# Optimization experiments

Hardware: AMD Instinct MI355X
Metric: run time of the kernel (lower is better)

The kernel has to match this reference:

```python
import jax, jax.numpy as jnp
import numpy as np

N, D, K = 8192, 2048, 10000
EPS = 1e-12
COMMITMENT_COST = 0.25


def _l2_normalize(v, axis):
    # matches torch F.normalize(p=2): v / max(||v||, eps)
    n = jnp.linalg.norm(v, axis=axis, keepdims=True)
    return v / jnp.maximum(n, EPS)


def setup_inputs() -> dict:
    key = jax.random.key(0)
    kx, kw = jax.random.split(key)
    x = jax.random.normal(kx, (N, D), dtype=jnp.float32)
    # nn.Embedding weight initialized uniform(0, 3) per the module
    weight = jax.random.uniform(kw, (K, D), dtype=jnp.float32, minval=0.0, maxval=3.0)
    return {"x": x, "weight": weight}


def reference(x, weight):
    # --- get_code_indices ---
    xn = _l2_normalize(x, axis=1)          # [N, D]
    wn = _l2_normalize(weight, axis=1)     # [K, D]
    # ||xn||^2 + ||wn||^2 - 2 xn . wn  -> [N, K]
    distances = (
        jnp.sum(xn * xn, axis=1, keepdims=True)
        + jnp.sum(wn * wn, axis=1)
        - 2.0 * jnp.matmul(xn, wn.T)
    )
    encoding_indices = jnp.argmin(distances, axis=1)  # [N]
    # --- quantize (gathers the UN-normalized codebook, as in the module) ---
    quantized = weight[encoding_indices]              # [N, D]
    # --- training losses ---
    q_latent_loss = jnp.mean((quantized - jax.lax.stop_gradient(x)) ** 2)
    e_latent_loss = jnp.mean((x - jax.lax.stop_gradient(quantized)) ** 2)
    loss = q_latent_loss + COMMITMENT_COST * e_latent_loss
    # straight-through estimator
    quantized = x + jax.lax.stop_gradient(quantized - x)
    return quantized, loss, encoding_indices
```

## Files before the change

kernel.cpp:

```cpp
#include <hip/hip_runtime.h>
#include <math.h>

typedef unsigned short ushort_t;
typedef short short8 __attribute__((ext_vector_type(8)));
typedef float f32x4  __attribute__((ext_vector_type(4)));

#define N_ROWS 8192
#define D_DIM  2048
#define K_CODES 10000
#define EPSF   1e-12f

#define BMT 256
#define BKT 64
#define NT_K 32
#define MTILES 32
#define NTILES 40
#define NGROUP 320

#define BAND_ADD  2e-5f
#define FBIG 1e30f

__device__ __forceinline__ unsigned short f2bf(float f) {
  unsigned u = __float_as_uint(f);
  unsigned r = (u + 0x7fffu + ((u >> 16) & 1u)) >> 16;
  return (unsigned short)r;
}
__device__ __forceinline__ float bf2f(unsigned short h) {
  return __uint_as_float(((unsigned)h) << 16);
}

__device__ __forceinline__ void stage16(const ushort_t* g, ushort_t* l) {
  __builtin_amdgcn_global_load_lds(
      (const __attribute__((address_space(1))) unsigned int*)g,
      (__attribute__((address_space(3))) unsigned int*)l, 16, 0, 0);
}

__device__ __forceinline__ float block_reduce_sum(float v) {
  #pragma unroll
  for (int o = 32; o > 0; o >>= 1) v += __shfl_down(v, o, 64);
  __shared__ float ls[4];
  int lane = threadIdx.x & 63;
  int wid  = threadIdx.x >> 6;
  if (lane == 0) ls[wid] = v;
  __syncthreads();
  v = (threadIdx.x < 4) ? ls[threadIdx.x] : 0.0f;
  if (wid == 0) {
    v += __shfl_down(v, 2, 64);
    v += __shfl_down(v, 1, 64);
  }
  __syncthreads();
  return v;
}

__global__ __launch_bounds__(256) void norm_hi_kernel(
    const float* __restrict__ src, ushort_t* __restrict__ hi,
    float* __restrict__ sq_out, float* __restrict__ inv_out,
    float* __restrict__ hn_out, float* __restrict__ ln_out)
{
  int row = blockIdx.x;
  int tid = threadIdx.x;
  const float* rp = src + (size_t)row * D_DIM;
  float4 v0 = *(const float4*)(rp + tid * 8);
  float4 v1 = *(const float4*)(rp + tid * 8 + 4);
  float s = v0.x*v0.x + v0.y*v0.y + v0.z*v0.z + v0.w*v0.w
          + v1.x*v1.x + v1.y*v1.y + v1.z*v1.z + v1.w*v1.w;
  s = block_reduce_sum(s);
  __shared__ float sh_inv;
  if (tid == 0) sh_inv = 1.0f / fmaxf(sqrtf(s), EPSF);
  __syncthreads();
  float inv = sh_inv;

  float xs[8] = {v0.x, v0.y, v0.z, v0.w, v1.x, v1.y, v1.z, v1.w};
  unsigned short hb[8];
  float t = 0.0f, th = 0.0f, tl = 0.0f;
  #pragma unroll
  for (int i = 0; i < 8; ++i) {
    float xn = xs[i] * inv;
    t += xn * xn;
    unsigned short h = f2bf(xn);
    hb[i] = h;
    float hf = bf2f(h);
    th += hf * hf;
    float l = xn - hf;
    tl += l * l;
  }
  *(short8*)(hi + (size_t)row * D_DIM + tid * 8) = *(short8*)hb;
  t  = block_reduce_sum(t);
  if (tid == 0) sq_out[row] = t;
  th = block_reduce_sum(th);
  if (tid == 0) hn_out[row] = sqrtf(th);
  tl = block_reduce_sum(tl);
  if (tid == 0) { ln_out[row] = sqrtf(tl); inv_out[row] = inv; }
}

__global__ __launch_bounds__(256) void wmax_kernel(
    const float* __restrict__ whn, const float* __restrict__ wln,
    float* __restrict__ wmax_out)
{
  int tid = threadIdx.x;
  float mh = 0.0f, ml = 0.0f;
  for (int k = tid; k < K_CODES; k += 256) {
    mh = fmaxf(mh, whn[k]);
    ml = fmaxf(ml, wln[k]);
  }
  __shared__ float sh[256], sl[256];
  sh[tid] = mh; sl[tid] = ml;
  __syncthreads();
  #pragma unroll
  for (int o = 128; o > 0; o >>= 1) {
    if (tid < o) {
      sh[tid] = fmaxf(sh[tid], sh[tid + o]);
      sl[tid] = fmaxf(sl[tid], sl[tid + o]);
    }
    __syncthreads();
  }
  if (tid == 0) { wmax_out[0] = sh[0]; wmax_out[1] = sl[0]; }
}

#define LEXLT(da, ia, db, ib) ((da) < (db) || ((da) == (db) && (ia) < (ib)))


#define READ_A(mh) { \
  _Pragma("unroll") for (int mi = 0; mi < 4; ++mi) { \
    af[mi][0] = *(const short8*)(aP0 + bo + (mh)*8192 + mi*1024); \
    af[mi][1] = *(const short8*)(aP1 + bo + (mh)*8192 + mi*1024); } }

#define READ_B(nh, DST) { \
  _Pragma("unroll") for (int ni = 0; ni < 2; ++ni) { \
    DST[ni][0] = *(const short8*)(bP0 + bo + (nh)*8192 + ni*1024); \
    DST[ni][1] = *(const short8*)(bP1 + bo + (nh)*8192 + ni*1024); } }

#define MFMA_Q(mh, nh, BF) { \
  _Pragma("unroll") for (int mi = 0; mi < 4; ++mi) \
  _Pragma("unroll") for (int ni = 0; ni < 2; ++ni) \
  _Pragma("unroll") for (int kc = 0; kc < 2; ++kc) \
    acc[(mh)*4+mi][(nh)*2+ni] = __builtin_amdgcn_mfma_f32_16x16x32_bf16( \
        af[mi][kc], BF[ni][kc], acc[(mh)*4+mi][(nh)*2+ni], 0, 0, 0); }

#define STAGE_A(NB, HH, KKO) { \
  stage16(Ah + (size_t)(row0 + (HH)*128 + prow0) * D_DIM + (KKO) + lsl, \
          &lA[0][0] + (NB)*16384 + (HH)*8192 + c0*512); \
  stage16(Ah + (size_t)(row0 + (HH)*128 + prow1) * D_DIM + (KKO) + lsl, \
          &lA[0][0] + (NB)*16384 + (HH)*8192 + c0*512 + 512); }

#define STAGE_B(NB, HH, KKO) { \
  int r0_ = col0 + (HH)*128 + prow0; r0_ = r0_ < K_CODES ? r0_ : K_CODES - 1; \
  int r1_ = col0 + (HH)*128 + prow1; r1_ = r1_ < K_CODES ? r1_ : K_CODES - 1; \
  stage16(Bh + (size_t)r0_ * D_DIM + (KKO) + lsl, \
          &lB[0][0] + (NB)*16384 + (HH)*8192 + c0*512); \
  stage16(Bh + (size_t)r1_ * D_DIM + (KKO) + lsl, \
          &lB[0][0] + (NB)*16384 + (HH)*8192 + c0*512 + 512); }

__global__ __launch_bounds__(512, 2) void dist_top2_kernel(
    const ushort_t* __restrict__ Ah, const ushort_t* __restrict__ Bh,
    const float* __restrict__ wsq,
    float* __restrict__ p1d, int* __restrict__ p1i, float* __restrict__ p2d)
{
  __shared__ ushort_t lA[2][16384];
  __shared__ ushort_t lB[2][16384];

  const int tid  = threadIdx.x;
  const int lane = tid & 63;
  const int w8   = tid >> 6;
  const int wr   = w8 >> 2;
  const int wc   = w8 & 3;
  const int t16  = lane & 15;
  const int h4   = lane >> 4;

  int bid = blockIdx.x;
  int xcd = bid & 7, l = bid >> 3;
  int ch = l >> 5;
  int wl = l & 31;
  const int mtile = (xcd & 1) * 16 + (wl & 15);
  const int ntile = (xcd >> 1) * 10 + ch * 2 + (wl >> 4);
  const int row0 = mtile * BMT;
  const int col0 = ntile * BMT;

  const int sub  = lane >> 3;
  const int lsl  = ((lane & 7) ^ sub) * 8;
  const int c0   = w8 * 2;
  const int prow0 = c0 * 8 + sub;
  const int prow1 = prow0 + 8;

  const int rA = wr * 64 + t16;
  const ushort_t* aP0 = &lA[0][rA * 64 + ((h4     ^ (rA & 7)) * 8)];
  const ushort_t* aP1 = &lA[0][rA * 64 + (((4+h4) ^ (rA & 7)) * 8)];
  const int rB = wc * 32 + t16;
  const ushort_t* bP0 = &lB[0][rB * 64 + ((h4     ^ (rB & 7)) * 8)];
  const ushort_t* bP1 = &lB[0][rB * 64 + (((4+h4) ^ (rB & 7)) * 8)];

  f32x4 acc[8][4];
  #pragma unroll
  for (int m = 0; m < 8; ++m)
    #pragma unroll
    for (int n = 0; n < 4; ++n) acc[m][n] = (f32x4){0.f, 0.f, 0.f, 0.f};

  STAGE_A(0, 0, 0);
  STAGE_B(0, 0, 0);
  STAGE_B(0, 1, 0);
  STAGE_A(0, 1, 0);
  __syncthreads();

  short8 af[4][2], bfr0[2][2], bfr1[2][2];

  for (int kt = 0; kt < NT_K; ++kt) {
    const int bo   = (kt & 1) * 16384;
    const int nb   = (kt + 1) & 1;
    const bool hn  = (kt + 1 < NT_K);
    const int kk   = (kt + 1) * BKT;

    if (hn) {
      STAGE_A(nb, 0, kk);
      STAGE_B(nb, 0, kk);
      STAGE_B(nb, 1, kk);
      STAGE_A(nb, 1, kk);
    }

    READ_A(0);
    READ_B(0, bfr0);
    __builtin_amdgcn_s_setprio(1);
    MFMA_Q(0, 0, bfr0);
    __builtin_amdgcn_s_setprio(0);
    READ_B(1, bfr1);
    __builtin_amdgcn_s_setprio(1);
    MFMA_Q(0, 1, bfr1);
    __builtin_amdgcn_s_setprio(0);
    READ_A(1);
    __builtin_amdgcn_s_setprio(1);
    MFMA_Q(1, 1, bfr1);
    MFMA_Q(1, 0, bfr0);
    __builtin_amdgcn_s_setprio(0);

    __syncthreads();
  }

  float wsqr[4]; int colr[4];
  #pragma unroll
  for (int n = 0; n < 4; ++n) {
    int col = col0 + ((n & 2) ? 128 : 0) + wc * 32 + ((n & 1) ? 16 : 0) + t16;
    colr[n] = col;
    wsqr[n] = (col < K_CODES) ? wsq[col] : FBIG * 10.0f;
  }
  #pragma unroll
  for (int m = 0; m < 8; ++m) {
    int rloc = ((m & 4) ? 128 : 0) + wr * 64 + (m & 3) * 16 + h4 * 4;
    #pragma unroll
    for (int j = 0; j < 4; ++j) {
      #pragma unroll
      for (int half = 0; half < 2; ++half) {
        int na = half * 2, nb2 = na + 1;
        float da = wsqr[na]  - 2.0f * acc[m][na][j];  int ia = colr[na];
        float db = wsqr[nb2] - 2.0f * acc[m][nb2][j]; int ib = colr[nb2];
        float d1, d2; int i1;
        if (LEXLT(db, ib, da, ia)) { d1 = db; i1 = ib; d2 = da; }
        else                       { d1 = da; i1 = ia; d2 = db; }
        #pragma unroll
        for (int off = 1; off < 16; off <<= 1) {
          float od1 = __shfl_xor(d1, off, 64);
          int   oi1 = __shfl_xor(i1, off, 64);
          float od2 = __shfl_xor(d2, off, 64);
          if (LEXLT(od1, oi1, d1, i1)) { d2 = fminf(d1, od2); d1 = od1; i1 = oi1; }
          else                         { d2 = fminf(od1, d2); }
        }
        if (t16 == 0) {
          int grow = row0 + rloc + j;
          int gid = ntile * 8 + half * 4 + wc;
          size_t o = (size_t)grow * NGROUP + gid;
          p1d[o] = d1; p1i[o] = i1; p2d[o] = d2;
        }
      }
    }
  }
}

__global__ __launch_bounds__(256) void refine_kernel(
    const float* __restrict__ x, const float* __restrict__ w,
    const float* __restrict__ xsq, const float* __restrict__ xinv,
    const float* __restrict__ xhn, const float* __restrict__ xln,
    const float* __restrict__ wsq, const float* __restrict__ winv,
    const float* __restrict__ whn, const float* __restrict__ wln,
    const float* __restrict__ wmax,
    const float* __restrict__ p1d, const int* __restrict__ p1i,
    const float* __restrict__ p2d,
    int* __restrict__ idx_out, float* __restrict__ idxf_out)
{
  const int wv   = threadIdx.x >> 6;
  const int lane = threadIdx.x & 63;
  const int row  = blockIdx.x * 4 + wv;

  const float xs = xsq[row], xh = xhn[row], xl = xln[row];
  const float whm = wmax[0], wlm = wmax[1];
  const float eps_max = 2.0f * (xl * whm + xh * wlm + xl * wlm) + BAND_ADD;

  float gd1[5], gd2[5], geps[5];
  int   gi1[5];
  float tmin = FBIG;
  float bmind = FBIG; int bmink = 0x7fffffff;
  #pragma unroll
  for (int s = 0; s < 5; ++s) {
    size_t o = (size_t)row * NGROUP + lane + 64 * s;
    float d1 = p1d[o]; int i1 = p1i[o]; float d2 = p2d[o];
    int is = i1 < K_CODES ? i1 : K_CODES - 1;
    float e1 = 2.0f * (xl * whn[is] + xh * wln[is] + xl * wln[is]) + BAND_ADD;
    gd1[s] = d1; gi1[s] = i1; gd2[s] = d2; geps[s] = e1;
    tmin = fminf(tmin, d1 + e1);
    if (d1 < bmind || (d1 == bmind && i1 < bmink)) { bmind = d1; bmink = i1; }
  }
  #pragma unroll
  for (int off = 1; off < 64; off <<= 1) tmin = fminf(tmin, __shfl_xor(tmin, off, 64));
  const float T = tmin;

  #pragma unroll
  for (int off = 1; off < 64; off <<= 1) {
    float od = __shfl_xor(bmind, off, 64);
    int   ok = __shfl_xor(bmink, off, 64);
    if (od < bmind || (od == bmind && ok < bmink)) { bmind = od; bmink = ok; }
  }
  const int kfirst = bmink;

  unsigned long long ms[5], mc[5];
  int ncand = 0, nscan = 0;
  #pragma unroll
  for (int s = 0; s < 5; ++s) {
    bool scan = (gd2[s] - eps_max <= T);
    bool cand = !scan && (gd1[s] - geps[s] <= T);
    ms[s] = __ballot(scan); mc[s] = __ballot(cand);
    nscan += __popcll(ms[s]); ncand += __popcll(mc[s]);
  }
  if (nscan == 0 && ncand == 1) {
    if (lane == 0) { idx_out[row] = kfirst; idxf_out[row] = (float)kfirst; }
    return;
  }

  const float4* xr4 = (const float4*)(x + (size_t)row * D_DIM);
  const float xiv = xinv[row];
  float4 xv[8];
  #pragma unroll
  for (int j = 0; j < 8; ++j) {
    float4 v = xr4[lane + 64 * j];
    v.x *= xiv; v.y *= xiv; v.z *= xiv; v.w *= xiv;
    xv[j] = v;
  }

  float bd = INFINITY; int bi = 0x7fffffff;
  auto refine = [&](int k) {
    const float4* wr4 = (const float4*)(w + (size_t)k * D_DIM);
    const float wiv = winv[k];
    float a = 0.0f;
    #pragma unroll
    for (int j = 0; j < 8; ++j) {
      float4 wvv = wr4[lane + 64 * j];
      a += xv[j].x * (wvv.x * wiv) + xv[j].y * (wvv.y * wiv)
         + xv[j].z * (wvv.z * wiv) + xv[j].w * (wvv.w * wiv);
    }
    #pragma unroll
    for (int off = 32; off > 0; off >>= 1) a += __shfl_xor(a, off, 64);
    float df = (xs + wsq[k]) - 2.0f * a;
    if (df < bd || (df == bd && k < bi)) { bd = df; bi = k; }
  };

  if (kfirst < K_CODES) refine(kfirst);

  #pragma unroll
  for (int s = 0; s < 5; ++s) {
    unsigned long long m = mc[s];
    while (m) {
      int lsrc = __ffsll(m) - 1; m &= m - 1;
      int k = __shfl(gi1[s], lsrc, 64);
      if (k == kfirst || k >= K_CODES) continue;
      float a1d = __shfl(gd1[s],  lsrc, 64);
      float a1e = __shfl(geps[s], lsrc, 64);
      if (a1d - a1e <= bd + BAND_ADD) refine(k);
    }
    m = ms[s];
    while (m) {
      int lsrc = __ffsll(m) - 1; m &= m - 1;
      float a2d = __shfl(gd2[s], lsrc, 64);
      if (a2d - eps_max > bd + BAND_ADD) continue;
      int k0 = (lsrc + 64 * s) * 32;
      for (int kk = 0; kk < 32; ++kk) {
        int k = k0 + kk;
        if (k < K_CODES) refine(k);
      }
    }
  }

  if (lane == 0) { idx_out[row] = bi; idxf_out[row] = (float)bi; }
}

__global__ __launch_bounds__(256) void gather_kernel(
    const float* __restrict__ x, const float* __restrict__ w,
    const int* __restrict__ idx, float* __restrict__ out,
    float* __restrict__ lpart)
{
  int row = blockIdx.x;
  int tid = threadIdx.x;
  int id = idx[row];
  const float4* wr_ = (const float4*)(w + (size_t)id * D_DIM);
  const float4* xr  = (const float4*)(x + (size_t)row * D_DIM);
  float4* outr = (float4*)(out + (size_t)row * D_DIM);
  float s = 0.0f;
  #pragma unroll
  for (int t = 0; t < 2; ++t) {
    int e = tid + t * 256;
    float4 wv = wr_[e], xv = xr[e];
    outr[e] = wv;
    float d0 = wv.x - xv.x, d1 = wv.y - xv.y, d2 = wv.z - xv.z, d3 = wv.w - xv.w;
    s += d0 * d0 + d1 * d1 + d2 * d2 + d3 * d3;
  }
  s = block_reduce_sum(s);
  if (tid == 0) lpart[row] = s;
}

__global__ __launch_bounds__(256) void loss_kernel(const float* __restrict__ lpart,
                                                   float* __restrict__ loss_out)
{
  int tid = threadIdx.x;
  double s = 0.0;
  for (int t = tid; t < N_ROWS; t += 256) s += (double)lpart[t];
  __shared__ double sd[256];
  sd[tid] = s;
  __syncthreads();
  #pragma unroll
  for (int o = 128; o > 0; o >>= 1) {
    if (tid < o) sd[tid] += sd[tid + o];
    __syncthreads();
  }
  if (tid == 0)
    loss_out[0] = (float)(1.25 * sd[0] / (double)((size_t)N_ROWS * (size_t)D_DIM));
}

extern "C" void kernel_launch(void* const* d_in, const int* in_sizes, int n_in,
                              void* d_out, int out_size, void* d_ws, size_t ws_size,
                              hipStream_t stream) {
  const float* x = (const float*)d_in[0];
  const float* w = (const float*)d_in[1];
  float* out = (float*)d_out;
  char*  ws  = (char*)d_ws;

  size_t off = 0;
  auto alloc = [&](size_t bytes) {
    size_t o = off;
    off = (off + bytes + 255) & ~(size_t)255;
    return o;
  };
  const size_t szA1 = (size_t)N_ROWS * D_DIM * 2;
  const size_t szB1 = (size_t)K_CODES * D_DIM * 2;
  const size_t szP  = (size_t)NGROUP * N_ROWS * 4;

  ushort_t* Bh = (ushort_t*)(ws + alloc(szB1));
  float* wsq  = (float*)(ws + alloc((size_t)K_CODES * 4));
  float* winv = (float*)(ws + alloc((size_t)K_CODES * 4));
  float* whn  = (float*)(ws + alloc((size_t)K_CODES * 4));
  float* wln  = (float*)(ws + alloc((size_t)K_CODES * 4));
  float* wmax = (float*)(ws + alloc(2 * 4));
  float* xsq  = (float*)(ws + alloc((size_t)N_ROWS * 4));
  float* xinv = (float*)(ws + alloc((size_t)N_ROWS * 4));
  float* xhn  = (float*)(ws + alloc((size_t)N_ROWS * 4));
  float* xln  = (float*)(ws + alloc((size_t)N_ROWS * 4));
  float* p1d  = (float*)(ws + alloc(szP));
  int*   p1i  = (int*)  (ws + alloc(szP));
  float* p2d  = (float*)(ws + alloc(szP));
  int*   idx  = (int*)  (ws + alloc((size_t)N_ROWS * 4));
  float* lpart = (float*)(ws + alloc((size_t)N_ROWS * 4));

  ushort_t* Ahp;
  if (ws_size >= off + szA1) {
    Ahp = (ushort_t*)(ws + alloc(szA1));
  } else {
    Ahp = (ushort_t*)out;
  }

  float* loss_out = out + (size_t)N_ROWS * D_DIM;
  float* idxf_out = loss_out + 1;

  norm_hi_kernel<<<N_ROWS, 256, 0, stream>>>(x, Ahp, xsq, xinv, xhn, xln);
  norm_hi_kernel<<<K_CODES, 256, 0, stream>>>(w, Bh, wsq, winv, whn, wln);
  wmax_kernel<<<1, 256, 0, stream>>>(whn, wln, wmax);
  dist_top2_kernel<<<MTILES * NTILES, 512, 0, stream>>>(
      Ahp, Bh, wsq, p1d, p1i, p2d);
  refine_kernel<<<N_ROWS / 4, 256, 0, stream>>>(
      x, w, xsq, xinv, xhn, xln, wsq, winv, whn, wln, wmax,
      p1d, p1i, p2d, idx, idxf_out);
  gather_kernel<<<N_ROWS, 256, 0, stream>>>(x, w, idx, out, lpart);
  loss_kernel<<<1, 256, 0, stream>>>(lpart, loss_out);
}
```

Baseline: 785.5 us.

## Replace 256x256 double-buffered GEMM tile with simple single-buffered 128x128 tile

The distance GEMM kernel moves from 256x256 tiles with 512 threads, double-buffered LDS, setprio interleaving and an XCD-aware block swizzle to 128x128 tiles with 256 threads, a single LDS buffer and two barriers per k-step. The candidate output layout is remapped so that each 128-column tile still yields four groups, keeping NGROUP at 320. The intent is to raise occupancy and the number of blocks, but the change drops the global-load/compute overlap, lowers the arithmetic intensity per tile, and removes the L2-locality swizzle.

```diff
diff --git a/kernel.cpp b/kernel.cpp
--- a/kernel.cpp
+++ b/kernel.cpp
@@ -10,11 +10,11 @@
 #define K_CODES 10000
 #define EPSF   1e-12f
 
-#define BMT 256
+#define BMT 128
 #define BKT 64
-#define NT_K 32
-#define MTILES 32
-#define NTILES 40
+#define KT_N 32
+#define MT 64
+#define NT 80
 #define NGROUP 320
 
 #define BAND_ADD  2e-5f
@@ -120,137 +120,91 @@
 #define LEXLT(da, ia, db, ib) ((da) < (db) || ((da) == (db) && (ia) < (ib)))
 
 
-#define READ_A(mh) { \
-  _Pragma("unroll") for (int mi = 0; mi < 4; ++mi) { \
-    af[mi][0] = *(const short8*)(aP0 + bo + (mh)*8192 + mi*1024); \
-    af[mi][1] = *(const short8*)(aP1 + bo + (mh)*8192 + mi*1024); } }
-
-#define READ_B(nh, DST) { \
-  _Pragma("unroll") for (int ni = 0; ni < 2; ++ni) { \
-    DST[ni][0] = *(const short8*)(bP0 + bo + (nh)*8192 + ni*1024); \
-    DST[ni][1] = *(const short8*)(bP1 + bo + (nh)*8192 + ni*1024); } }
-
-#define MFMA_Q(mh, nh, BF) { \
-  _Pragma("unroll") for (int mi = 0; mi < 4; ++mi) \
-  _Pragma("unroll") for (int ni = 0; ni < 2; ++ni) \
-  _Pragma("unroll") for (int kc = 0; kc < 2; ++kc) \
-    acc[(mh)*4+mi][(nh)*2+ni] = __builtin_amdgcn_mfma_f32_16x16x32_bf16( \
-        af[mi][kc], BF[ni][kc], acc[(mh)*4+mi][(nh)*2+ni], 0, 0, 0); }
-
-#define STAGE_A(NB, HH, KKO) { \
-  stage16(Ah + (size_t)(row0 + (HH)*128 + prow0) * D_DIM + (KKO) + lsl, \
-          &lA[0][0] + (NB)*16384 + (HH)*8192 + c0*512); \
-  stage16(Ah + (size_t)(row0 + (HH)*128 + prow1) * D_DIM + (KKO) + lsl, \
-          &lA[0][0] + (NB)*16384 + (HH)*8192 + c0*512 + 512); }
-
-#define STAGE_B(NB, HH, KKO) { \
-  int r0_ = col0 + (HH)*128 + prow0; r0_ = r0_ < K_CODES ? r0_ : K_CODES - 1; \
-  int r1_ = col0 + (HH)*128 + prow1; r1_ = r1_ < K_CODES ? r1_ : K_CODES - 1; \
-  stage16(Bh + (size_t)r0_ * D_DIM + (KKO) + lsl, \
-          &lB[0][0] + (NB)*16384 + (HH)*8192 + c0*512); \
-  stage16(Bh + (size_t)r1_ * D_DIM + (KKO) + lsl, \
-          &lB[0][0] + (NB)*16384 + (HH)*8192 + c0*512 + 512); }
-
-__global__ __launch_bounds__(512, 2) void dist_top2_kernel(
+#define STAGE_A(KKO) { \
+  _Pragma("unroll") for (int j = 0; j < 4; ++j) \
+    stage16(Ah + (size_t)(row0 + w4*32 + j*8 + sub) * D_DIM + (KKO) + lsl, \
+            lA + w4*2048 + j*512); }
+
+#define STAGE_B(KKO) { \
+  _Pragma("unroll") for (int j = 0; j < 4; ++j) { \
+    int rr = col0 + w4*32 + j*8 + sub; rr = rr < K_CODES ? rr : K_CODES - 1; \
+    stage16(Bh + (size_t)rr * D_DIM + (KKO) + lsl, \
+            lB + w4*2048 + j*512); } }
+
+#define COMPUTE_HALF(AP, BP) { \
+  _Pragma("unroll") for (int m = 0; m < 4; ++m) \
+    af[m] = *(const short8*)((AP) + m*1024); \
+  _Pragma("unroll") for (int n = 0; n < 4; ++n) \
+    bf[n] = *(const short8*)((BP) + n*1024); \
+  _Pragma("unroll") for (int m = 0; m < 4; ++m) \
+  _Pragma("unroll") for (int n = 0; n < 4; ++n) \
+    acc[m][n] = __builtin_amdgcn_mfma_f32_16x16x32_bf16( \
+        af[m], bf[n], acc[m][n], 0, 0, 0); }
+
+__global__ __launch_bounds__(256, 4) void dist_top2_kernel(
     const ushort_t* __restrict__ Ah, const ushort_t* __restrict__ Bh,
     const float* __restrict__ wsq,
     float* __restrict__ p1d, int* __restrict__ p1i, float* __restrict__ p2d)
 {
-  __shared__ ushort_t lA[2][16384];
-  __shared__ ushort_t lB[2][16384];
+  __shared__ ushort_t lA[8192];
+  __shared__ ushort_t lB[8192];
 
   const int tid  = threadIdx.x;
   const int lane = tid & 63;
-  const int w8   = tid >> 6;
-  const int wr   = w8 >> 2;
-  const int wc   = w8 & 3;
+  const int w4   = tid >> 6;
+  const int wm   = w4 >> 1;
+  const int wn   = w4 & 1;
   const int t16  = lane & 15;
   const int h4   = lane >> 4;
 
-  int bid = blockIdx.x;
-  int xcd = bid & 7, l = bid >> 3;
-  int ch = l >> 5;
-  int wl = l & 31;
-  const int mtile = (xcd & 1) * 16 + (wl & 15);
-  const int ntile = (xcd >> 1) * 10 + ch * 2 + (wl >> 4);
+  const int mtile = blockIdx.x & 63;
+  const int ntile = blockIdx.x >> 6;
   const int row0 = mtile * BMT;
   const int col0 = ntile * BMT;
 
-  const int sub  = lane >> 3;
-  const int lsl  = ((lane & 7) ^ sub) * 8;
-  const int c0   = w8 * 2;
-  const int prow0 = c0 * 8 + sub;
-  const int prow1 = prow0 + 8;
-
-  const int rA = wr * 64 + t16;
-  const ushort_t* aP0 = &lA[0][rA * 64 + ((h4     ^ (rA & 7)) * 8)];
-  const ushort_t* aP1 = &lA[0][rA * 64 + (((4+h4) ^ (rA & 7)) * 8)];
-  const int rB = wc * 32 + t16;
-  const ushort_t* bP0 = &lB[0][rB * 64 + ((h4     ^ (rB & 7)) * 8)];
-  const ushort_t* bP1 = &lB[0][rB * 64 + (((4+h4) ^ (rB & 7)) * 8)];
-
-  f32x4 acc[8][4];
-  #pragma unroll
-  for (int m = 0; m < 8; ++m)
+  const int sub = lane >> 3;
+  const int lsl = ((lane & 7) ^ sub) * 8;
+
+  const ushort_t* aP0 = &lA[(wm*64 + t16)*64 + ((h4       ^ (t16 & 7)) * 8)];
+  const ushort_t* aP1 = &lA[(wm*64 + t16)*64 + (((4 + h4) ^ (t16 & 7)) * 8)];
+  const ushort_t* bP0 = &lB[(wn*64 + t16)*64 + ((h4       ^ (t16 & 7)) * 8)];
+  const ushort_t* bP1 = &lB[(wn*64 + t16)*64 + (((4 + h4) ^ (t16 & 7)) * 8)];
+
+  f32x4 acc[4][4];
+  #pragma unroll
+  for (int m = 0; m < 4; ++m)
     #pragma unroll
     for (int n = 0; n < 4; ++n) acc[m][n] = (f32x4){0.f, 0.f, 0.f, 0.f};
 
-  STAGE_A(0, 0, 0);
-  STAGE_B(0, 0, 0);
-  STAGE_B(0, 1, 0);
-  STAGE_A(0, 1, 0);
-  __syncthreads();
-
-  short8 af[4][2], bfr0[2][2], bfr1[2][2];
-
-  for (int kt = 0; kt < NT_K; ++kt) {
-    const int bo   = (kt & 1) * 16384;
-    const int nb   = (kt + 1) & 1;
-    const bool hn  = (kt + 1 < NT_K);
-    const int kk   = (kt + 1) * BKT;
-
-    if (hn) {
-      STAGE_A(nb, 0, kk);
-      STAGE_B(nb, 0, kk);
-      STAGE_B(nb, 1, kk);
-      STAGE_A(nb, 1, kk);
-    }
-
-    READ_A(0);
-    READ_B(0, bfr0);
-    __builtin_amdgcn_s_setprio(1);
-    MFMA_Q(0, 0, bfr0);
-    __builtin_amdgcn_s_setprio(0);
-    READ_B(1, bfr1);
-    __builtin_amdgcn_s_setprio(1);
-    MFMA_Q(0, 1, bfr1);
-    __builtin_amdgcn_s_setprio(0);
-    READ_A(1);
-    __builtin_amdgcn_s_setprio(1);
-    MFMA_Q(1, 1, bfr1);
-    MFMA_Q(1, 0, bfr0);
-    __builtin_amdgcn_s_setprio(0);
-
+  short8 af[4], bf[4];
+
+  for (int kt = 0; kt < KT_N; ++kt) {
+    const int kk = kt * BKT;
+    STAGE_A(kk);
+    STAGE_B(kk);
     __syncthreads();
+    COMPUTE_HALF(aP0, bP0);
+    COMPUTE_HALF(aP1, bP1);
+    __syncthreads();
   }
 
   float wsqr[4]; int colr[4];
   #pragma unroll
   for (int n = 0; n < 4; ++n) {
-    int col = col0 + ((n & 2) ? 128 : 0) + wc * 32 + ((n & 1) ? 16 : 0) + t16;
+    int col = col0 + wn * 64 + n * 16 + t16;
     colr[n] = col;
     wsqr[n] = (col < K_CODES) ? wsq[col] : FBIG * 10.0f;
   }
   #pragma unroll
-  for (int m = 0; m < 8; ++m) {
-    int rloc = ((m & 4) ? 128 : 0) + wr * 64 + (m & 3) * 16 + h4 * 4;
+  for (int m = 0; m < 4; ++m) {
+    int rloc = wm * 64 + m * 16 + h4 * 4;
     #pragma unroll
     for (int j = 0; j < 4; ++j) {
       #pragma unroll
       for (int half = 0; half < 2; ++half) {
-        int na = half * 2, nb2 = na + 1;
-        float da = wsqr[na]  - 2.0f * acc[m][na][j];  int ia = colr[na];
-        float db = wsqr[nb2] - 2.0f * acc[m][nb2][j]; int ib = colr[nb2];
+        int na = half * 2, nb = na + 1;
+        float da = wsqr[na] - 2.0f * acc[m][na][j]; int ia = colr[na];
+        float db = wsqr[nb] - 2.0f * acc[m][nb][j]; int ib = colr[nb];
         float d1, d2; int i1;
         if (LEXLT(db, ib, da, ia)) { d1 = db; i1 = ib; d2 = da; }
         else                       { d1 = da; i1 = ia; d2 = db; }
@@ -264,7 +218,7 @@
         }
         if (t16 == 0) {
           int grow = row0 + rloc + j;
-          int gid = ntile * 8 + half * 4 + wc;
+          int gid = ntile * 4 + wn * 2 + half;
           size_t o = (size_t)grow * NGROUP + gid;
           p1d[o] = d1; p1i[o] = i1; p2d[o] = d2;
         }
@@ -477,7 +431,7 @@
   norm_hi_kernel<<<N_ROWS, 256, 0, stream>>>(x, Ahp, xsq, xinv, xhn, xln);
   norm_hi_kernel<<<K_CODES, 256, 0, stream>>>(w, Bh, wsq, winv, whn, wln);
   wmax_kernel<<<1, 256, 0, stream>>>(whn, wln, wmax);
-  dist_top2_kernel<<<MTILES * NTILES, 512, 0, stream>>>(
+  dist_top2_kernel<<<MT * NT, 256, 0, stream>>>(
       Ahp, Bh, wsq, p1d, p1i, p2d);
   refine_kernel<<<N_ROWS / 4, 256, 0, stream>>>(
       x, w, xsq, xinv, xhn, xln, wsq, winv, whn, wln, wmax,
```

Measured after the change: 729.4 us. 7.1% less time.
